# Optimization experiments

Hardware: AMD Instinct MI355X
Metric: run time of the kernel (lower is better)

The kernel has to match this reference:

```python
import jax, jax.numpy as jnp
import numpy as np

FIRE_RATE = 0.5
ANGLE = 0.0

def _sobel_kernels(angle=ANGLE):
    dx = np.outer([1, 2, 1], [-1, 0, 1]) / 8.0
    dy = dx.T
    c = np.cos(angle * np.pi / 180.0)
    s = np.sin(angle * np.pi / 180.0)
    w1 = (c * dx - s * dy).astype(np.float32)
    w2 = (s * dx + c * dy).astype(np.float32)
    # torch applies conv after transpose(1,3) so its spatial axes are (W,H);
    # transposing kernels makes our NHWC conv over (H,W) match exactly.
    return jnp.asarray(w1.T), jnp.asarray(w2.T)

def _depthwise3x3(x, w):
    # x: [B,H,W,C], w: [3,3] shared across all C channels (groups=C)
    C = x.shape[-1]
    k = jnp.tile(w[:, :, None, None], (1, 1, 1, C))  # [3,3,1,C] HWIO
    return jax.lax.conv_general_dilated(
        x, k, window_strides=(1, 1), padding='SAME',
        dimension_numbers=('NHWC', 'HWIO', 'NHWC'),
        feature_group_count=C)

def setup_inputs() -> dict:
    key = jax.random.key(0)
    k1, k2, k3 = jax.random.split(key, 3)
    B, H, W, C, HID = 8, 256, 256, 16, 128
    x = jax.random.uniform(k1, (B, H, W, C), dtype=jnp.float32)
    # xavier-uniform-like init for fc0/fc1
    lim0 = float(np.sqrt(6.0 / (3 * C + HID)))
    lim1 = float(np.sqrt(6.0 / (HID + C)))
    W0 = jax.random.uniform(k2, (HID, 3 * C), minval=-lim0, maxval=lim0, dtype=jnp.float32)
    b0 = jnp.zeros((HID,), dtype=jnp.float32)
    W1 = jax.random.uniform(k3, (C, HID), minval=-lim1, maxval=lim1, dtype=jnp.float32)
    return {'x': x, 'W0': W0, 'b0': b0, 'W1': W1, 'steps': 2}

def reference(x, W0, b0, W1, steps):
    w1, w2 = _sobel_kernels()
    key = jax.random.key(42)
    for step in range(steps):
        # perceive: identity + two depthwise sobel filters -> [B,H,W,3C]
        y = jnp.concatenate([x, _depthwise3x3(x, w1), _depthwise3x3(x, w2)], axis=-1)
        # per-cell MLP
        h = jax.nn.relu(jnp.einsum('bhwk,ok->bhwo', y, W0) + b0)
        dx = jnp.einsum('bhwo,co->bhwc', h, W1)
        # stochastic fire-rate mask [B,H,W,1]
        mk = jax.random.fold_in(key, step)
        mask = (jax.random.uniform(mk, dx.shape[:3] + (1,)) > FIRE_RATE).astype(dx.dtype)
        new = x + dx * mask
        # only channels 3: are updated (first 3 channels stay fixed)
        x = jnp.concatenate([x[..., :3], new[..., 3:]], axis=-1)
    return x
```

## Files before the change

kernel.cpp:

```cpp
#include <hip/hip_runtime.h>
#include <hip/hip_bf16.h>
#include <stdint.h>


#define NB 8
#define NH 256
#define NW 256
#define NC 16
#define TH 4
#define TW 16
#define WOFF 65536

typedef __attribute__((ext_vector_type(8))) short short8;
typedef __attribute__((ext_vector_type(4))) float floatx4;

__host__ __device__ inline void tf2x32(uint32_t k0, uint32_t k1,
                                       uint32_t x0, uint32_t x1,
                                       uint32_t& o0, uint32_t& o1) {
  const uint32_t ks2 = k0 ^ k1 ^ 0x1BD11BDAu;
  x0 += k0; x1 += k1;
#define RL(v, d) (((v) << (d)) | ((v) >> (32 - (d))))
#define R4(a, b, c, d)                          \
  x0 += x1; x1 = RL(x1, a); x1 ^= x0;           \
  x0 += x1; x1 = RL(x1, b); x1 ^= x0;           \
  x0 += x1; x1 = RL(x1, c); x1 ^= x0;           \
  x0 += x1; x1 = RL(x1, d); x1 ^= x0;
  R4(13, 15, 26, 6);  x0 += k1;  x1 += ks2 + 1u;
  R4(17, 29, 16, 24); x0 += ks2; x1 += k0 + 2u;
  R4(13, 15, 26, 6);  x0 += k0;  x1 += k1 + 3u;
  R4(17, 29, 16, 24); x0 += k1;  x1 += ks2 + 4u;
  R4(13, 15, 26, 6);  x0 += ks2; x1 += k0 + 5u;
#undef R4
#undef RL
  o0 = x0; o1 = x1;
}

__device__ inline short bfr(float x) {
  __hip_bfloat16 h = __float2bfloat16(x);
  return *reinterpret_cast<short*>(&h);
}

__global__ __launch_bounds__(64) void ca_prep(
    const float* __restrict__ W0, const float* __restrict__ b0,
    const float* __restrict__ W1, short* __restrict__ wbuf) {
  const int lane = threadIdx.x;
  const int c15 = lane & 15;
  const int g = lane >> 4;
  short8* wf = reinterpret_cast<short8*>(wbuf);

  const float s0 = (g < 2) ? 1.0f : 0.125f;
#pragma unroll
  for (int n = 0; n < 8; ++n) {
    const int o = 16 * n + c15;
    const float* p = W0 + o * 48 + 8 * g;
    const floatx4 v0 = *reinterpret_cast<const floatx4*>(p);
    const floatx4 v1 = *reinterpret_cast<const floatx4*>(p + 4);
    short8 f;
    f[0] = bfr(v0.x * s0); f[1] = bfr(v0.y * s0);
    f[2] = bfr(v0.z * s0); f[3] = bfr(v0.w * s0);
    f[4] = bfr(v1.x * s0); f[5] = bfr(v1.y * s0);
    f[6] = bfr(v1.z * s0); f[7] = bfr(v1.w * s0);
    wf[(2 * n) * 64 + lane] = f;
    short8 f1;
    if (g < 2) {
      const float* p1 = W0 + o * 48 + 32 + 8 * g;
      const floatx4 u0 = *reinterpret_cast<const floatx4*>(p1);
      const floatx4 u1 = *reinterpret_cast<const floatx4*>(p1 + 4);
      f1[0] = bfr(u0.x * 0.125f); f1[1] = bfr(u0.y * 0.125f);
      f1[2] = bfr(u0.z * 0.125f); f1[3] = bfr(u0.w * 0.125f);
      f1[4] = bfr(u1.x * 0.125f); f1[5] = bfr(u1.y * 0.125f);
      f1[6] = bfr(u1.z * 0.125f); f1[7] = bfr(u1.w * 0.125f);
    } else {
#pragma unroll
      for (int j = 0; j < 8; ++j) f1[j] = 0;
      if (g == 2) f1[0] = bfr(b0[o]);
    }
    wf[(2 * n + 1) * 64 + lane] = f1;
  }
#pragma unroll
  for (int s = 0; s < 4; ++s) {
    const float* p = W1 + c15 * 128 + 32 * s + 4 * g;
    const floatx4 v0 = *reinterpret_cast<const floatx4*>(p);
    const floatx4 v1 = *reinterpret_cast<const floatx4*>(p + 16);
    short8 f;
    f[0] = bfr(v0.x); f[1] = bfr(v0.y); f[2] = bfr(v0.z); f[3] = bfr(v0.w);
    f[4] = bfr(v1.x); f[5] = bfr(v1.y); f[6] = bfr(v1.z); f[7] = bfr(v1.w);
    wf[(16 + s) * 64 + lane] = f;
  }
}

template <bool PRE>
__global__ __launch_bounds__(64, 2) void ca_step(
    const float* __restrict__ xin, float* __restrict__ xout,
    const float* __restrict__ W0, const float* __restrict__ b0,
    const float* __restrict__ W1, const short* __restrict__ wfrag,
    uint32_t fk0, uint32_t fk1) {
  __shared__ float xs[6 * 18 * 16];

  const int tid = threadIdx.x;
  const int bt = blockIdx.x;
  const int wt = bt & 15;
  const int ht8 = (bt >> 4) & 31;
  const int b = bt >> 9;
  const int h0 = ht8 * 8;
  const int w0 = wt * TW;

  const int lane = tid;
  const int c15 = lane & 15;
  const int g = lane >> 4;

  auto xsaddr = [&](int row, int col, int chunk) -> floatx4* {
    const int off = (row * 18 + col) * 64 + ((chunk ^ ((col >> 1) & 3)) << 4);
    return reinterpret_cast<floatx4*>(reinterpret_cast<char*>(xs) + off);
  };

  short8 w0f[8][2];
  short8 w1f[4];
  if constexpr (PRE) {
    const short8* wf = reinterpret_cast<const short8*>(wfrag);
#pragma unroll
    for (int n = 0; n < 8; ++n) {
      w0f[n][0] = wf[(2 * n) * 64 + lane];
      w0f[n][1] = wf[(2 * n + 1) * 64 + lane];
    }
#pragma unroll
    for (int s = 0; s < 4; ++s) w1f[s] = wf[(16 + s) * 64 + lane];
  } else {
    const float s0 = (g < 2) ? 1.0f : 0.125f;
#pragma unroll
    for (int n = 0; n < 8; ++n) {
      const int o = 16 * n + c15;
      const float* p = W0 + o * 48 + 8 * g;
      const floatx4 v0 = *reinterpret_cast<const floatx4*>(p);
      const floatx4 v1 = *reinterpret_cast<const floatx4*>(p + 4);
      short8 f;
      f[0] = bfr(v0.x * s0); f[1] = bfr(v0.y * s0);
      f[2] = bfr(v0.z * s0); f[3] = bfr(v0.w * s0);
      f[4] = bfr(v1.x * s0); f[5] = bfr(v1.y * s0);
      f[6] = bfr(v1.z * s0); f[7] = bfr(v1.w * s0);
      w0f[n][0] = f;
      short8 f1;
      if (g < 2) {
        const float* p1 = W0 + o * 48 + 32 + 8 * g;
        const floatx4 u0 = *reinterpret_cast<const floatx4*>(p1);
        const floatx4 u1 = *reinterpret_cast<const floatx4*>(p1 + 4);
        f1[0] = bfr(u0.x * 0.125f); f1[1] = bfr(u0.y * 0.125f);
        f1[2] = bfr(u0.z * 0.125f); f1[3] = bfr(u0.w * 0.125f);
        f1[4] = bfr(u1.x * 0.125f); f1[5] = bfr(u1.y * 0.125f);
        f1[6] = bfr(u1.z * 0.125f); f1[7] = bfr(u1.w * 0.125f);
      } else {
#pragma unroll
        for (int j = 0; j < 8; ++j) f1[j] = 0;
        if (g == 2) f1[0] = bfr(b0[o]);
      }
      w0f[n][1] = f1;
    }
#pragma unroll
    for (int s = 0; s < 4; ++s) {
      const float* p = W1 + c15 * 128 + 32 * s + 4 * g;
      const floatx4 v0 = *reinterpret_cast<const floatx4*>(p);
      const floatx4 v1 = *reinterpret_cast<const floatx4*>(p + 16);
      short8 f;
      f[0] = bfr(v0.x); f[1] = bfr(v0.y); f[2] = bfr(v0.z); f[3] = bfr(v0.w);
      f[4] = bfr(v1.x); f[5] = bfr(v1.y); f[6] = bfr(v1.z); f[7] = bfr(v1.w);
      w1f[s] = f;
    }
  }

  const int cc = 2 * (g & 1);
  const bool lo = (g < 2);

  constexpr float WA[8] = {-1.f, -2.f, -1.f, 0.f, 0.f, 1.f, 2.f, 1.f};
  constexpr float WB[8] = {-1.f, 0.f, 1.f, -2.f, 2.f, -1.f, 0.f, 1.f};

#pragma unroll 1
  for (int t2 = 0; t2 < 2; ++t2) {
    const int h0t = h0 + TH * t2;

    __syncthreads();

    for (int f = tid; f < 6 * 18 * 4; f += 64) {
      const int row = f / 72;
      const int rem = f - row * 72;
      const int col = rem >> 2;
      const int q = rem & 3;
      const int gh = h0t - 1 + row;
      const int gw = w0 - 1 + col;
      floatx4 v = {0.f, 0.f, 0.f, 0.f};
      if ((unsigned)gh < (unsigned)NH && (unsigned)gw < (unsigned)NW)
        v = *reinterpret_cast<const floatx4*>(
            xin + (((size_t)b * NH + gh) * NW + gw) * NC + 4 * q);
      *xsaddr(row, col, q) = v;
    }

    uint64_t mball;
    {
      const int cellg = (b * NH + h0t + (lane >> 4)) * NW + w0 + c15;
      uint32_t r0, r1;
      tf2x32(fk0, fk1, 0u, (uint32_t)cellg, r0, r1);
      const uint32_t bits = r0 ^ r1;
      const float u = __uint_as_float((bits >> 9) | 0x3F800000u) - 1.0f;
      mball = __ballot(u > 0.5f);
    }
    __syncthreads();

#pragma unroll
    for (int mt = 0; mt < 4; ++mt) {
      const int r = 1 + mt;
      const int col = 1 + c15;

      const floatx4 xc0 = *xsaddr(r, col, cc);
      const floatx4 xc1 = *xsaddr(r, col, cc + 1);

      float sob[8];
#pragma unroll
      for (int j = 0; j < 8; ++j) sob[j] = 0.f;
      int t = 0;
#pragma unroll
      for (int dh = -1; dh <= 1; ++dh)
#pragma unroll
        for (int dw = -1; dw <= 1; ++dw) {
          if (dh == 0 && dw == 0) continue;
          const floatx4 v0 = *xsaddr(r + dh, col + dw, cc);
          const floatx4 v1 = *xsaddr(r + dh, col + dw, cc + 1);
          const float w = lo ? WB[t] : WA[t];
          ++t;
          sob[0] += w * v0.x; sob[1] += w * v0.y;
          sob[2] += w * v0.z; sob[3] += w * v0.w;
          sob[4] += w * v1.x; sob[5] += w * v1.y;
          sob[6] += w * v1.z; sob[7] += w * v1.w;
        }

      const float xcv[8] = {xc0.x, xc0.y, xc0.z, xc0.w,
                            xc1.x, xc1.y, xc1.z, xc1.w};
      short8 a0, a1;
#pragma unroll
      for (int j = 0; j < 8; ++j) {
        const short sb = bfr(sob[j]);
        a0[j] = lo ? bfr(xcv[j]) : sb;
        a1[j] = lo ? sb : (short)0;
      }
      if (g == 2) a1[0] = bfr(1.0f);

      floatx4 acc[8];
#pragma unroll
      for (int n = 0; n < 8; ++n) acc[n] = floatx4{0.f, 0.f, 0.f, 0.f};
#pragma unroll
      for (int n = 0; n < 8; ++n)
        acc[n] = __builtin_amdgcn_mfma_f32_16x16x32_bf16(w0f[n][0], a0, acc[n], 0, 0, 0);
#pragma unroll
      for (int n = 0; n < 8; ++n)
        acc[n] = __builtin_amdgcn_mfma_f32_16x16x32_bf16(w0f[n][1], a1, acc[n], 0, 0, 0);

      floatx4 acc2 = {0.f, 0.f, 0.f, 0.f};
#pragma unroll
      for (int s = 0; s < 4; ++s) {
        short8 b2;
#pragma unroll
        for (int j = 0; j < 8; ++j)
          b2[j] = bfr(fmaxf(acc[2 * s + (j >> 2)][j & 3], 0.f));
        acc2 = __builtin_amdgcn_mfma_f32_16x16x32_bf16(w1f[s], b2, acc2, 0, 0, 0);
      }

      const floatx4 xv = *xsaddr(r, col, g);
      const float mk = (float)((mball >> (16 * mt + c15)) & 1ull);
      const float mk03 = (g == 0) ? 0.f : mk;
      floatx4 ov;
      ov.x = xv.x + acc2.x * mk03;
      ov.y = xv.y + acc2.y * mk03;
      ov.z = xv.z + acc2.z * mk03;
      ov.w = xv.w + acc2.w * mk;
      const size_t cellg = ((size_t)(b * NH + h0t + mt)) * NW + w0 + c15;
      *reinterpret_cast<floatx4*>(xout + cellg * NC + 4 * g) = ov;
    }
  }
}

extern "C" void kernel_launch(void* const* d_in, const int* in_sizes, int n_in,
                              void* d_out, int out_size, void* d_ws, size_t ws_size,
                              hipStream_t stream) {
  const float* x  = (const float*)d_in[0];
  const float* W0 = (const float*)d_in[1];
  const float* b0 = (const float*)d_in[2];
  const float* W1 = (const float*)d_in[3];
  float* out = (float*)d_out;

  const size_t tmp_bytes = (size_t)NB * NH * NW * NC * 4;
  const bool pre = ws_size >= (size_t)WOFF + tmp_bytes;
  short* wbuf = (short*)d_ws;
  float* tmp = pre ? (float*)((char*)d_ws + WOFF) : (float*)d_ws;

  uint32_t fa0, fa1, fb0, fb1;
  tf2x32(0u, 42u, 0u, 0u, fa0, fa1);
  tf2x32(0u, 42u, 0u, 1u, fb0, fb1);

  dim3 grid(NB * (NH / 8) * (NW / TW)), block(64);
  if (pre) {
    ca_prep<<<1, 64, 0, stream>>>(W0, b0, W1, wbuf);
    ca_step<true><<<grid, block, 0, stream>>>(x, tmp, W0, b0, W1, wbuf, fa0, fa1);
    ca_step<true><<<grid, block, 0, stream>>>(tmp, out, W0, b0, W1, wbuf, fb0, fb1);
  } else {
    ca_step<false><<<grid, block, 0, stream>>>(x, tmp, W0, b0, W1, nullptr, fa0, fa1);
    ca_step<false><<<grid, block, 0, stream>>>(tmp, out, W0, b0, W1, nullptr, fb0, fb1);
  }
}
```

Baseline: 69.93 us.

## Double-buffer halo tiles with register prefetch and taller per-block row span

Each block now processes 16 rows in four 4-row phases instead of 8 rows in two. The next phase's halo tile is prefetched into registers while the current phase computes, then written into a second shared-memory buffer. This is meant to hide global load latency and spread the weight-fragment setup over more work. The prep kernel is also split across 20 blocks so it runs in parallel. In exchange there are half as many blocks, higher register pressure from the 7 staged vectors, and double the shared memory.

After: 65.55 us. 6.3% less time.

```diff
diff --git a/kernel.cpp b/kernel.cpp
--- a/kernel.cpp
+++ b/kernel.cpp
@@ -7,8 +7,6 @@
 #define NH 256
 #define NW 256
 #define NC 16
-#define TH 4
-#define TW 16
 #define WOFF 65536
 
 typedef __attribute__((ext_vector_type(8))) short short8;
@@ -46,47 +44,43 @@
   const int lane = threadIdx.x;
   const int c15 = lane & 15;
   const int g = lane >> 4;
-  short8* wf = reinterpret_cast<short8*>(wbuf);
-
-  const float s0 = (g < 2) ? 1.0f : 0.125f;
-#pragma unroll
-  for (int n = 0; n < 8; ++n) {
+  const int fi = blockIdx.x;
+  short8 f;
+  if (fi < 16) {
+    const int n = fi >> 1;
     const int o = 16 * n + c15;
-    const float* p = W0 + o * 48 + 8 * g;
-    const floatx4 v0 = *reinterpret_cast<const floatx4*>(p);
-    const floatx4 v1 = *reinterpret_cast<const floatx4*>(p + 4);
-    short8 f;
-    f[0] = bfr(v0.x * s0); f[1] = bfr(v0.y * s0);
-    f[2] = bfr(v0.z * s0); f[3] = bfr(v0.w * s0);
-    f[4] = bfr(v1.x * s0); f[5] = bfr(v1.y * s0);
-    f[6] = bfr(v1.z * s0); f[7] = bfr(v1.w * s0);
-    wf[(2 * n) * 64 + lane] = f;
-    short8 f1;
-    if (g < 2) {
-      const float* p1 = W0 + o * 48 + 32 + 8 * g;
-      const floatx4 u0 = *reinterpret_cast<const floatx4*>(p1);
-      const floatx4 u1 = *reinterpret_cast<const floatx4*>(p1 + 4);
-      f1[0] = bfr(u0.x * 0.125f); f1[1] = bfr(u0.y * 0.125f);
-      f1[2] = bfr(u0.z * 0.125f); f1[3] = bfr(u0.w * 0.125f);
-      f1[4] = bfr(u1.x * 0.125f); f1[5] = bfr(u1.y * 0.125f);
-      f1[6] = bfr(u1.z * 0.125f); f1[7] = bfr(u1.w * 0.125f);
+    if ((fi & 1) == 0) {
+      const float s0 = (g < 2) ? 1.0f : 0.125f;
+      const float* p = W0 + o * 48 + 8 * g;
+      const floatx4 v0 = *reinterpret_cast<const floatx4*>(p);
+      const floatx4 v1 = *reinterpret_cast<const floatx4*>(p + 4);
+      f[0] = bfr(v0.x * s0); f[1] = bfr(v0.y * s0);
+      f[2] = bfr(v0.z * s0); f[3] = bfr(v0.w * s0);
+      f[4] = bfr(v1.x * s0); f[5] = bfr(v1.y * s0);
+      f[6] = bfr(v1.z * s0); f[7] = bfr(v1.w * s0);
     } else {
-#pragma unroll
-      for (int j = 0; j < 8; ++j) f1[j] = 0;
-      if (g == 2) f1[0] = bfr(b0[o]);
-    }
-    wf[(2 * n + 1) * 64 + lane] = f1;
-  }
-#pragma unroll
-  for (int s = 0; s < 4; ++s) {
-    const float* p = W1 + c15 * 128 + 32 * s + 4 * g;
-    const floatx4 v0 = *reinterpret_cast<const floatx4*>(p);
-    const floatx4 v1 = *reinterpret_cast<const floatx4*>(p + 16);
-    short8 f;
-    f[0] = bfr(v0.x); f[1] = bfr(v0.y); f[2] = bfr(v0.z); f[3] = bfr(v0.w);
-    f[4] = bfr(v1.x); f[5] = bfr(v1.y); f[6] = bfr(v1.z); f[7] = bfr(v1.w);
-    wf[(16 + s) * 64 + lane] = f;
-  }
+      if (g < 2) {
+        const float* p1 = W0 + o * 48 + 32 + 8 * g;
+        const floatx4 u0 = *reinterpret_cast<const floatx4*>(p1);
+        const floatx4 u1 = *reinterpret_cast<const floatx4*>(p1 + 4);
+        f[0] = bfr(u0.x * 0.125f); f[1] = bfr(u0.y * 0.125f);
+        f[2] = bfr(u0.z * 0.125f); f[3] = bfr(u0.w * 0.125f);
+        f[4] = bfr(u1.x * 0.125f); f[5] = bfr(u1.y * 0.125f);
+        f[6] = bfr(u1.z * 0.125f); f[7] = bfr(u1.w * 0.125f);
+      } else {
+#pragma unroll
+        for (int j = 0; j < 8; ++j) f[j] = 0;
+        if (g == 2) f[0] = bfr(b0[o]);
+      }
+    }
+  } else {
+    const int s = fi - 16;
+    const float* p = W1 + c15 * 128;
+#pragma unroll
+    for (int j = 0; j < 8; ++j)
+      f[j] = bfr(p[32 * s + 16 * (j >> 2) + 4 * g + (j & 3)]);
+  }
+  reinterpret_cast<short8*>(wbuf)[fi * 64 + lane] = f;
 }
 
 template <bool PRE>
@@ -95,23 +89,23 @@
     const float* __restrict__ W0, const float* __restrict__ b0,
     const float* __restrict__ W1, const short* __restrict__ wfrag,
     uint32_t fk0, uint32_t fk1) {
-  __shared__ float xs[6 * 18 * 16];
+  __shared__ float xs[2][6 * 18 * 16];
 
   const int tid = threadIdx.x;
   const int bt = blockIdx.x;
   const int wt = bt & 15;
-  const int ht8 = (bt >> 4) & 31;
-  const int b = bt >> 9;
-  const int h0 = ht8 * 8;
-  const int w0 = wt * TW;
+  const int ht16 = (bt >> 4) & 15;
+  const int b = bt >> 8;
+  const int h0 = ht16 * 16;
+  const int w0 = wt * 16;
 
   const int lane = tid;
   const int c15 = lane & 15;
   const int g = lane >> 4;
 
-  auto xsaddr = [&](int row, int col, int chunk) -> floatx4* {
+  auto xsaddr = [&](float* base, int row, int col, int chunk) -> floatx4* {
     const int off = (row * 18 + col) * 64 + ((chunk ^ ((col >> 1) & 3)) << 4);
-    return reinterpret_cast<floatx4*>(reinterpret_cast<char*>(xs) + off);
+    return reinterpret_cast<floatx4*>(reinterpret_cast<char*>(base) + off);
   };
 
   short8 w0f[8][2];
@@ -157,12 +151,11 @@
     }
 #pragma unroll
     for (int s = 0; s < 4; ++s) {
-      const float* p = W1 + c15 * 128 + 32 * s + 4 * g;
-      const floatx4 v0 = *reinterpret_cast<const floatx4*>(p);
-      const floatx4 v1 = *reinterpret_cast<const floatx4*>(p + 16);
+      const float* p = W1 + c15 * 128;
       short8 f;
-      f[0] = bfr(v0.x); f[1] = bfr(v0.y); f[2] = bfr(v0.z); f[3] = bfr(v0.w);
-      f[4] = bfr(v1.x); f[5] = bfr(v1.y); f[6] = bfr(v1.z); f[7] = bfr(v1.w);
+#pragma unroll
+      for (int j = 0; j < 8; ++j)
+        f[j] = bfr(p[32 * s + 16 * (j >> 2) + 4 * g + (j & 3)]);
       w1f[s] = f;
     }
   }
@@ -173,24 +166,55 @@
   constexpr float WA[8] = {-1.f, -2.f, -1.f, 0.f, 0.f, 1.f, 2.f, 1.f};
   constexpr float WB[8] = {-1.f, 0.f, 1.f, -2.f, 2.f, -1.f, 0.f, 1.f};
 
+  auto load_ph = [&](int h0t, floatx4* stg) {
+#pragma unroll
+    for (int i = 0; i < 7; ++i) {
+      const int f = lane + 64 * i;
+      floatx4 v = {0.f, 0.f, 0.f, 0.f};
+      if (f < 432) {
+        const int row = f / 72;
+        const int rem = f - row * 72;
+        const int col = rem >> 2;
+        const int q = rem & 3;
+        const int gh = h0t - 1 + row;
+        const int gw = w0 - 1 + col;
+        if ((unsigned)gh < (unsigned)NH && (unsigned)gw < (unsigned)NW)
+          v = *reinterpret_cast<const floatx4*>(
+              xin + (((size_t)b * NH + gh) * NW + gw) * NC + 4 * q);
+      }
+      stg[i] = v;
+    }
+  };
+  auto write_ph = [&](float* buf, const floatx4* stg) {
+#pragma unroll
+    for (int i = 0; i < 7; ++i) {
+      const int f = lane + 64 * i;
+      if (f < 432) {
+        const int row = f / 72;
+        const int rem = f - row * 72;
+        const int col = rem >> 2;
+        const int q = rem & 3;
+        *xsaddr(buf, row, col, q) = stg[i];
+      }
+    }
+  };
+
+  {
+    floatx4 s0[7];
+    load_ph(h0, s0);
+    write_ph(reinterpret_cast<float*>(xs[0]), s0);
+  }
+  __syncthreads();
+
+  int cur = 0;
 #pragma unroll 1
-  for (int t2 = 0; t2 < 2; ++t2) {
-    const int h0t = h0 + TH * t2;
-
-    __syncthreads();
-
-    for (int f = tid; f < 6 * 18 * 4; f += 64) {
-      const int row = f / 72;
-      const int rem = f - row * 72;
-      const int col = rem >> 2;
-      const int q = rem & 3;
-      const int gh = h0t - 1 + row;
-      const int gw = w0 - 1 + col;
-      floatx4 v = {0.f, 0.f, 0.f, 0.f};
-      if ((unsigned)gh < (unsigned)NH && (unsigned)gw < (unsigned)NW)
-        v = *reinterpret_cast<const floatx4*>(
-            xin + (((size_t)b * NH + gh) * NW + gw) * NC + 4 * q);
-      *xsaddr(row, col, q) = v;
+  for (int t = 0; t < 4; ++t) {
+    const int h0t = h0 + 4 * t;
+
+    floatx4 stg[7];
+    if (t < 3) {
+      load_ph(h0t + 4, stg);
+      asm volatile("" ::: "memory");
     }
 
     uint64_t mball;
@@ -202,29 +226,30 @@
       const float u = __uint_as_float((bits >> 9) | 0x3F800000u) - 1.0f;
       mball = __ballot(u > 0.5f);
     }
-    __syncthreads();
+
+    float* xsb = reinterpret_cast<float*>(xs[cur]);
 
 #pragma unroll
     for (int mt = 0; mt < 4; ++mt) {
       const int r = 1 + mt;
       const int col = 1 + c15;
 
-      const floatx4 xc0 = *xsaddr(r, col, cc);
-      const floatx4 xc1 = *xsaddr(r, col, cc + 1);
+      const floatx4 xc0 = *xsaddr(xsb, r, col, cc);
+      const floatx4 xc1 = *xsaddr(xsb, r, col, cc + 1);
 
       float sob[8];
 #pragma unroll
       for (int j = 0; j < 8; ++j) sob[j] = 0.f;
-      int t = 0;
+      int t8 = 0;
 #pragma unroll
       for (int dh = -1; dh <= 1; ++dh)
 #pragma unroll
         for (int dw = -1; dw <= 1; ++dw) {
           if (dh == 0 && dw == 0) continue;
-          const floatx4 v0 = *xsaddr(r + dh, col + dw, cc);
-          const floatx4 v1 = *xsaddr(r + dh, col + dw, cc + 1);
-          const float w = lo ? WB[t] : WA[t];
-          ++t;
+          const floatx4 v0 = *xsaddr(xsb, r + dh, col + dw, cc);
+          const floatx4 v1 = *xsaddr(xsb, r + dh, col + dw, cc + 1);
+          const float w = lo ? WB[t8] : WA[t8];
+          ++t8;
           sob[0] += w * v0.x; sob[1] += w * v0.y;
           sob[2] += w * v0.z; sob[3] += w * v0.w;
           sob[4] += w * v1.x; sob[5] += w * v1.y;
@@ -262,7 +287,7 @@
         acc2 = __builtin_amdgcn_mfma_f32_16x16x32_bf16(w1f[s], b2, acc2, 0, 0, 0);
       }
 
-      const floatx4 xv = *xsaddr(r, col, g);
+      const floatx4 xv = *xsaddr(xsb, r, col, g);
       const float mk = (float)((mball >> (16 * mt + c15)) & 1ull);
       const float mk03 = (g == 0) ? 0.f : mk;
       floatx4 ov;
@@ -273,6 +298,13 @@
       const size_t cellg = ((size_t)(b * NH + h0t + mt)) * NW + w0 + c15;
       *reinterpret_cast<floatx4*>(xout + cellg * NC + 4 * g) = ov;
     }
+
+    if (t < 3) {
+      __syncthreads();
+      write_ph(reinterpret_cast<float*>(xs[cur ^ 1]), stg);
+      __syncthreads();
+      cur ^= 1;
+    }
   }
 }
 
@@ -294,9 +326,9 @@
   tf2x32(0u, 42u, 0u, 0u, fa0, fa1);
   tf2x32(0u, 42u, 0u, 1u, fb0, fb1);
 
-  dim3 grid(NB * (NH / 8) * (NW / TW)), block(64);
+  dim3 grid(NB * (NH / 16) * (NW / 16)), block(64);
   if (pre) {
-    ca_prep<<<1, 64, 0, stream>>>(W0, b0, W1, wbuf);
+    ca_prep<<<20, 64, 0, stream>>>(W0, b0, W1, wbuf);
     ca_step<true><<<grid, block, 0, stream>>>(x, tmp, W0, b0, W1, wbuf, fa0, fa1);
     ca_step<true><<<grid, block, 0, stream>>>(tmp, out, W0, b0, W1, wbuf, fb0, fb1);
   } else {
```
